# Kernel tuning notes

Hardware: AMD Instinct MI355X
Metric: run time of the kernel (lower is better)

## Reference

```python
import jax, jax.numpy as jnp
import numpy as np
import math

C = 256
NUM_CLASSES = 80
NUM_CONVS = 4
GROUPS = 32
LEVEL_SHAPES = [(100, 152), (50, 76), (25, 38), (13, 19), (7, 10)]
BATCH = 2


def conv2d(x, w, b):
    # x: [N,C,H,W], w: [O,I,3,3] -> SAME padding, stride 1
    y = jax.lax.conv_general_dilated(x, w, window_strides=(1, 1), padding='SAME',
                                     dimension_numbers=('NCHW', 'OIHW', 'NCHW'))
    return y + b[None, :, None, None]


def group_norm(x, w, b, groups=GROUPS, eps=1e-5):
    N, Ch, H, W = x.shape
    xg = x.reshape(N, groups, Ch // groups, H, W)
    mu = jnp.mean(xg, axis=(2, 3, 4), keepdims=True)
    var = jnp.var(xg, axis=(2, 3, 4), keepdims=True)
    xg = (xg - mu) * jax.lax.rsqrt(var + eps)
    x = xg.reshape(N, Ch, H, W)
    return x * w[None, :, None, None] + b[None, :, None, None]


def tower(x, cw, cb, gw, gb):
    for i in range(NUM_CONVS):
        x = jax.nn.relu(group_norm(conv2d(x, cw[i], cb[i]), gw[i], gb[i]))
    return x


def flatten_head(y, c):
    # [N, A*c, H, W] -> [N, H*W*A, c]  (matches view/permute/reshape in torch)
    N, AC, H, W = y.shape
    A = AC // c
    return y.reshape(N, A, c, H, W).transpose(0, 3, 4, 1, 2).reshape(N, H * W * A, c)


def setup_inputs() -> dict:
    key = jax.random.key(0)
    ks = iter(jax.random.split(key, 64))
    inp = {}
    for i, (h, w) in enumerate(LEVEL_SHAPES):
        inp[f"feat{i}"] = jax.random.normal(next(ks), (BATCH, C, h, w), jnp.float32)
    def cw(shape):  # conv weights init std=0.01 as in torch module
        return jax.random.normal(next(ks), shape, jnp.float32) * 0.01
    inp["cls_conv_w"] = cw((NUM_CONVS, C, C, 3, 3))
    inp["cls_conv_b"] = jnp.zeros((NUM_CONVS, C), jnp.float32)
    inp["cls_gn_w"] = jnp.ones((NUM_CONVS, C), jnp.float32)
    inp["cls_gn_b"] = jnp.zeros((NUM_CONVS, C), jnp.float32)
    inp["cls_out_w"] = cw((NUM_CLASSES, C, 3, 3))
    inp["cls_out_b"] = jnp.full((NUM_CLASSES,), -math.log(99.0), jnp.float32)  # prior prob 0.01
    inp["reg_conv_w"] = cw((NUM_CONVS, C, C, 3, 3))
    inp["reg_conv_b"] = jnp.zeros((NUM_CONVS, C), jnp.float32)
    inp["reg_gn_w"] = jnp.ones((NUM_CONVS, C), jnp.float32)
    inp["reg_gn_b"] = jnp.zeros((NUM_CONVS, C), jnp.float32)
    for name, oc in [("bbox", 4), ("ctr", 1), ("dim", 3), ("ori", 1), ("kp", 16), ("depth", 1)]:
        inp[f"{name}_w"] = cw((oc, C, 3, 3))
        inp[f"{name}_b"] = jnp.zeros((oc,), jnp.float32)
    return inp


def reference(feat0, feat1, feat2, feat3, feat4,
              cls_conv_w, cls_conv_b, cls_gn_w, cls_gn_b, cls_out_w, cls_out_b,
              reg_conv_w, reg_conv_b, reg_gn_w, reg_gn_b,
              bbox_w, bbox_b, ctr_w, ctr_b, dim_w, dim_b,
              ori_w, ori_b, kp_w, kp_b, depth_w, depth_b):
    feats = [feat0, feat1, feat2, feat3, feat4]
    cls_all, bbox_all, ctr_all, dim_all, ori_all, kp_all, depth_all = ([] for _ in range(7))
    for f in feats:
        cf = tower(f, cls_conv_w, cls_conv_b, cls_gn_w, cls_gn_b)
        cls_all.append(flatten_head(conv2d(cf, cls_out_w, cls_out_b), NUM_CLASSES))
        rf = tower(f, reg_conv_w, reg_conv_b, reg_gn_w, reg_gn_b)
        bbox_all.append(flatten_head(jax.nn.relu(conv2d(rf, bbox_w, bbox_b)), 4))
        ctr_all.append(flatten_head(conv2d(rf, ctr_w, ctr_b), 1))
        dim_all.append(flatten_head(conv2d(rf, dim_w, dim_b), 3))
        ori_all.append(flatten_head(conv2d(rf, ori_w, ori_b), 1))
        kp_all.append(flatten_head(conv2d(rf, kp_w, kp_b), 16))
        depth_all.append(flatten_head(conv2d(rf, depth_w, depth_b), 1))
    cat = lambda xs: jnp.concatenate(xs, axis=1)
    return (cat(cls_all), cat(bbox_all), cat(ctr_all), cat(dim_all),
            cat(ori_all), cat(kp_all), cat(depth_all))
```

## Files before the change

### kernel.cpp

```cpp
#include <hip/hip_runtime.h>
#include <stdint.h>

typedef unsigned short ushort_t;
typedef __bf16 bf16x8 __attribute__((ext_vector_type(8)));
typedef float f32x4 __attribute__((ext_vector_type(4)));

#define TOTAL_HW 20267
#define PTOT 21267

__constant__ int d_RB[26] = {3242720,3242720,3242720,3242720, 3404856, 3445390,3445390,3445390,
                             3566992, 3607526,3607526,3607526,3607526,3607526,3607526,3607526,3607526,
                             3607526,3607526,3607526,3607526,3607526,3607526,3607526,3607526, 4256070};
__constant__ int d_RM[26] = {4,4,4,4, 1, 3,3,3, 1, 16,16,16,16,16,16,16,16,16,16,16,16,16,16,16,16, 1};
__constant__ int d_RC[26] = {0,1,2,3, 0, 0,1,2, 0, 0,1,2,3,4,5,6,7,8,9,10,11,12,13,14,15, 0};

__constant__ int F_TC[6]   = {0,238,298,314,318,320};
__constant__ int F_TL[5]   = {119,30,8,2,1};
__constant__ int F_W[5]    = {152,76,38,19,10};
__constant__ int F_HW[5]   = {15200,3800,950,247,70};
__constant__ int F_PB[5]   = {0,15708,19764,20844,21159};
__constant__ int F_LOFF[5] = {0,15200,19000,19950,20197};
__constant__ int F_PC[6]   = {0,508,764,894,962,1000};
__constant__ int F_H[5]    = {100,50,25,13,7};

__device__ __forceinline__ ushort_t f2bf(float f) {
    union { float f; uint32_t i; } x; x.f = f;
    uint32_t r = x.i + 0x7fffu + ((x.i >> 16) & 1u);
    return (ushort_t)(r >> 16);
}
__device__ __forceinline__ float bf2f(ushort_t u) {
    union { uint32_t i; float f; } x; x.i = ((uint32_t)u) << 16; return x.f;
}
__device__ __forceinline__ void gld16(const ushort_t* g, ushort_t* lds) {
    __builtin_amdgcn_global_load_lds((const __attribute__((address_space(1))) void*)g,
                                     (__attribute__((address_space(3))) void*)lds, 16, 0, 0);
}

__global__ __launch_bounds__(256) void wtrans_towerall_k(const float* __restrict__ cw,
                                                         const float* __restrict__ rw,
                                                         ushort_t* __restrict__ dst)
{
    int id = blockIdx.x * 256 + threadIdx.x;
    int g = id >> 16;
    int oc = (id >> 8) & 255, ic = id & 255;
    const float* base = (g >= 4) ? rw : cw;
    int L = g & 3;
    const float* s = base + (size_t)L * 589824 + (size_t)(oc * 256 + ic) * 9;
    ushort_t* d = dst + (size_t)g * 589824 + oc * 256 + ic;
    #pragma unroll
    for (int t = 0; t < 9; t++) d[t * 65536] = f2bf(s[t]);
}
__global__ __launch_bounds__(256) void wtrans_cls_k(const float* __restrict__ src,
                                                    ushort_t* __restrict__ dst)
{
    int id = blockIdx.x * 256 + threadIdx.x;
    int oc = id >> 8, ic = id & 255;
    ushort_t* d = dst + oc * 256 + ic;
    if (oc < 80) {
        const float* s = src + (size_t)(oc * 256 + ic) * 9;
        #pragma unroll
        for (int t = 0; t < 9; t++) d[t * 32768] = f2bf(s[t]);
    } else {
        #pragma unroll
        for (int t = 0; t < 9; t++) d[t * 32768] = 0;
    }
}
__global__ __launch_bounds__(256) void wtrans_reg_k(
    const float* bbox_w, const float* ctr_w, const float* dim_w,
    const float* ori_w,  const float* kp_w,  const float* depth_w,
    const float* bbox_b, const float* ctr_b, const float* dim_b,
    const float* ori_b,  const float* kp_b,  const float* depth_b,
    ushort_t* __restrict__ dst, float* __restrict__ RegBias)
{
    int id = blockIdx.x * 256 + threadIdx.x;
    int oc = id >> 8, ic = id & 255;
    ushort_t* d = dst + oc * 256 + ic;
    if (oc < 26) {
        const float* s; int c;
        if (oc < 4)       { s = bbox_w;  c = oc; }
        else if (oc < 5)  { s = ctr_w;   c = 0; }
        else if (oc < 8)  { s = dim_w;   c = oc - 5; }
        else if (oc < 9)  { s = ori_w;   c = 0; }
        else if (oc < 25) { s = kp_w;    c = oc - 9; }
        else              { s = depth_w; c = 0; }
        const float* sp = s + (size_t)(c * 256 + ic) * 9;
        #pragma unroll
        for (int t = 0; t < 9; t++) d[t * 32768] = f2bf(sp[t]);
    } else {
        #pragma unroll
        for (int t = 0; t < 9; t++) d[t * 32768] = 0;
    }
    if (id < 26) {
        const float* b; int c;
        if (id < 4)       { b = bbox_b;  c = id; }
        else if (id < 5)  { b = ctr_b;   c = 0; }
        else if (id < 8)  { b = dim_b;   c = id - 5; }
        else if (id < 9)  { b = ori_b;   c = 0; }
        else if (id < 25) { b = kp_b;    c = id - 9; }
        else              { b = depth_b; c = 0; }
        RegBias[id] = b[c];
    }
}

__global__ __launch_bounds__(256) void pad_k(ushort_t* b0, ushort_t* b1, ushort_t* b2, ushort_t* b3)
{
    int u = blockIdx.x * 256 + threadIdx.x;
    if (u >= 256000) return;
    int chunk = u & 31; u >>= 5;
    int buf = u & 3; u >>= 2;
    int n = (u >= 1000) ? 1 : 0; int pidx = u - n * 1000;
    int l = 0;
    #pragma unroll
    for (int i = 1; i < 5; i++) if (pidx >= F_PC[i]) l = i;
    int q = pidx - F_PC[l];
    int W = F_W[l], H = F_H[l], Wp = W + 2;
    int py, px;
    if (q < Wp) { py = 0; px = q; }
    else if (q < 2 * Wp) { py = H + 1; px = q - Wp; }
    else { int q2 = q - 2 * Wp; py = 1 + (q2 >> 1); px = (q2 & 1) ? (Wp - 1) : 0; }
    ushort_t* base = b0;
    if (buf == 1) base = b1; else if (buf == 2) base = b2; else if (buf == 3) base = b3;
    *(uint4*)(base + ((size_t)n * PTOT + F_PB[l] + py * Wp + px) * 256 + chunk * 8) = uint4{0u,0u,0u,0u};
}

__global__ __launch_bounds__(256) void packF_k(
    const float* f0, const float* f1, const float* f2,
    const float* f3, const float* f4, ushort_t* __restrict__ S)
{
    __shared__ ushort_t tile[64][65];
    const int PCUM[6] = {0, 1904, 2384, 2504, 2536, 2552};
    const int PT[5]   = {238, 60, 15, 4, 2};
    int bid = blockIdx.x;
    int l = 0;
    #pragma unroll
    for (int i = 1; i < 5; i++) if (bid >= PCUM[i]) l = i;
    int r = bid - PCUM[l];
    int per_n = PT[l] * 4;
    int n = (r >= per_n) ? 1 : 0; r -= n * per_n;
    int pb = r >> 2, cb = r & 3;
    const float* fs = f0;
    if (l == 1) fs = f1; else if (l == 2) fs = f2; else if (l == 3) fs = f3; else if (l == 4) fs = f4;
    int HW = F_HW[l], W = F_W[l], Wp = W + 2;
    int p0 = pb * 64, c0 = cb * 64;
    int t = threadIdx.x;
    #pragma unroll
    for (int i = 0; i < 16; i++) {
        int idx = i * 256 + t; int cl = idx >> 6, pl = idx & 63;
        int p = p0 + pl; ushort_t v = 0;
        if (p < HW) v = f2bf(fs[(size_t)(n * 256 + c0 + cl) * HW + p]);
        tile[cl][pl] = v;
    }
    __syncthreads();
    ushort_t* ob = S + ((size_t)n * PTOT + F_PB[l]) * 256;
    #pragma unroll
    for (int i = 0; i < 16; i++) {
        int idx = i * 256 + t; int pl = idx >> 6, cl = idx & 63;
        int p = p0 + pl;
        if (p < HW) {
            int y = p / W, x = p - y * W;
            ob[((y + 1) * Wp + (x + 1)) * 256 + c0 + cl] = tile[cl][pl];
        }
    }
}

__global__ __launch_bounds__(512, 4) void convT_k(
    const ushort_t* __restrict__ srcC, const ushort_t* __restrict__ srcR,
    ushort_t* __restrict__ dstC, ushort_t* __restrict__ dstR,
    const ushort_t* __restrict__ wtAll,
    const float* __restrict__ biasC, const float* __restrict__ biasR,
    float* __restrict__ stats, int L)
{
    __shared__ __align__(16) ushort_t As[3][4096];
    __shared__ __align__(16) ushort_t Bs[3][4096];

    int gid = blockIdx.x;
    int xcd = gid & 7, idx = gid >> 3;
    int bid = xcd * 40 + (idx >> 2);
    int oc0 = (idx & 1) * 128;
    int tw = (idx >> 1) & 1;

    const ushort_t* src = tw ? srcR : srcC;
    ushort_t* dst = tw ? dstR : dstC;
    const ushort_t* wt = wtAll + (size_t)(tw * 4 + L) * 589824;
    const float* bias = (tw ? biasR : biasC) + L * 256;

    int l = 0;
    #pragma unroll
    for (int i = 1; i < 5; i++) if (bid >= F_TC[i]) l = i;
    int r = bid - F_TC[l];
    int tl = F_TL[l];
    int n = (r >= tl) ? 1 : 0; int tile = r - n * tl;
    int W = F_W[l], HW = F_HW[l], Wp = W + 2;
    int px0 = tile * 128;
    const ushort_t* sbase = src + ((size_t)n * PTOT + F_PB[l]) * 256;
    ushort_t* obase = dst + ((size_t)n * PTOT + F_PB[l]) * 256;

    int tid = threadIdx.x, wv = tid >> 6, ln = tid & 63;
    int wr = wv >> 2, wc = wv & 3;

    int aoff, boff;
    {
        int rloc = wv * 16 + (ln >> 2);
        int p = px0 + rloc; if (p > HW - 1) p = HW - 1;
        int y = p / W, x = p - y * W;
        int c = ((ln & 3) - (rloc >> 1)) & 3;
        aoff = ((y + 1) * Wp + (x + 1)) * 256 + c * 8;
        boff = (oc0 + rloc) * 256 + c * 8;
    }

    f32x4 acc[4][2];
    #pragma unroll
    for (int mi = 0; mi < 4; mi++)
        #pragma unroll
        for (int ni = 0; ni < 2; ni++) acc[mi][ni] = f32x4{0.f, 0.f, 0.f, 0.f};

    {
        int tapo = (-Wp - 1) * 256;
        gld16(sbase + aoff + tapo, &As[0][wv * 512]);
        gld16(wt + boff, &Bs[0][wv * 512]);
        asm volatile("" ::: "memory");
        gld16(sbase + aoff + tapo + 32, &As[1][wv * 512]);
        gld16(wt + 32 + boff, &Bs[1][wv * 512]);
    }

    #pragma unroll 3
    for (int it = 0; it < 72; ++it) {
        if (it < 71) {
            asm volatile("s_waitcnt vmcnt(2) lgkmcnt(0)\n\ts_barrier" ::: "memory");
        } else {
            asm volatile("s_waitcnt vmcnt(0) lgkmcnt(0)\n\ts_barrier" ::: "memory");
        }
        int nx = it + 2;
        if (nx < 72) {
            int tp = nx >> 3, kc = (nx & 7) << 5;
            int ky = tp / 3, kx = tp - ky * 3;
            int tapo = ((ky - 1) * Wp + (kx - 1)) * 256 + kc;
            const ushort_t* wtap = wt + tp * 65536 + kc;
            int bs = nx % 3;
            gld16(sbase + aoff + tapo, &As[bs][wv * 512]);
            gld16(wtap + boff, &Bs[bs][wv * 512]);
        }
        int b = it % 3;
        bf16x8 af[4], bg[2];
        #pragma unroll
        for (int mi = 0; mi < 4; mi++) {
            int rA = wr * 64 + mi * 16 + (ln & 15);
            int ch = ((ln >> 4) + (rA >> 1)) & 3;
            af[mi] = *(const bf16x8*)&As[b][rA * 32 + ch * 8];
        }
        #pragma unroll
        for (int ni = 0; ni < 2; ni++) {
            int rB = wc * 32 + ni * 16 + (ln & 15);
            int ch = ((ln >> 4) + (rB >> 1)) & 3;
            bg[ni] = *(const bf16x8*)&Bs[b][rB * 32 + ch * 8];
        }
        __builtin_amdgcn_s_setprio(1);
        #pragma unroll
        for (int mi = 0; mi < 4; mi++)
            #pragma unroll
            for (int ni = 0; ni < 2; ni++)
                acc[mi][ni] = __builtin_amdgcn_mfma_f32_16x16x32_bf16(af[mi], bg[ni], acc[mi][ni], 0, 0, 0);
        __builtin_amdgcn_s_setprio(0);
    }

    #pragma unroll
    for (int ni = 0; ni < 2; ni++) {
        int oc = oc0 + wc * 32 + ni * 16 + (ln & 15);
        float bv = bias[oc];
        float s = 0.f, q = 0.f;
        #pragma unroll
        for (int mi = 0; mi < 4; mi++) {
            int pb = px0 + wr * 64 + mi * 16 + ((ln >> 4) << 2);
            if (pb < HW) {
                int y = pb / W, x = pb - y * W;
                #pragma unroll
                for (int rr2 = 0; rr2 < 4; rr2++) {
                    int p = pb + rr2;
                    if (p < HW) {
                        float v = acc[mi][ni][rr2] + bv;
                        obase[((y + 1) * Wp + (x + 1)) * 256 + oc] = f2bf(v);
                        s += v; q += v * v;
                    }
                    x++; if (x == W) { x = 0; y++; }
                }
            }
        }
        s += __shfl_xor(s, 16, 64); q += __shfl_xor(q, 16, 64);
        s += __shfl_xor(s, 32, 64); q += __shfl_xor(q, 32, 64);
        s += __shfl_xor(s, 1, 64);  q += __shfl_xor(q, 1, 64);
        s += __shfl_xor(s, 2, 64);  q += __shfl_xor(q, 2, 64);
        s += __shfl_xor(s, 4, 64);  q += __shfl_xor(q, 4, 64);
        if (ln == 0 || ln == 8) {
            int g = (oc0 + wc * 32 + ni * 16 + (ln & 8)) >> 3;
            float* st = stats + (size_t)((tw * 4 + L) * 5 + l) * 128 + (n * 32 + g) * 2;
            atomicAdd(st, s); atomicAdd(st + 1, q);
        }
    }
}

__global__ __launch_bounds__(512, 4) void convH_k(
    const ushort_t* __restrict__ srcC, const ushort_t* __restrict__ srcR,
    const ushort_t* __restrict__ wtC, const ushort_t* __restrict__ wtR,
    const float* __restrict__ biasC, const float* __restrict__ biasR,
    float* __restrict__ outF)
{
    __shared__ __align__(16) ushort_t As[3][4096];
    __shared__ __align__(16) ushort_t Bs[3][4096];

    int gid = blockIdx.x;
    int xcd = gid & 7, idx = gid >> 3;
    int bid = xcd * 40 + (idx >> 1);
    int mode = idx & 1;

    const ushort_t* src = mode ? srcR : srcC;
    const ushort_t* wt  = mode ? wtR  : wtC;
    const float* bias   = mode ? biasR : biasC;

    int l = 0;
    #pragma unroll
    for (int i = 1; i < 5; i++) if (bid >= F_TC[i]) l = i;
    int r = bid - F_TC[l];
    int tl = F_TL[l];
    int n = (r >= tl) ? 1 : 0; int tile = r - n * tl;
    int W = F_W[l], HW = F_HW[l], Wp = W + 2;
    int px0 = tile * 128;
    const ushort_t* sbase = src + ((size_t)n * PTOT + F_PB[l]) * 256;

    int tid = threadIdx.x, wv = tid >> 6, ln = tid & 63;
    int wr = wv >> 2, wc = wv & 3;

    int aoff, boff;
    {
        int rloc = wv * 16 + (ln >> 2);
        int p = px0 + rloc; if (p > HW - 1) p = HW - 1;
        int y = p / W, x = p - y * W;
        int c = ((ln & 3) - (rloc >> 1)) & 3;
        aoff = ((y + 1) * Wp + (x + 1)) * 256 + c * 8;
        boff = rloc * 256 + c * 8;
    }

    f32x4 acc[4][2];
    #pragma unroll
    for (int mi = 0; mi < 4; mi++)
        #pragma unroll
        for (int ni = 0; ni < 2; ni++) acc[mi][ni] = f32x4{0.f, 0.f, 0.f, 0.f};

    {
        int tapo = (-Wp - 1) * 256;
        gld16(sbase + aoff + tapo, &As[0][wv * 512]);
        gld16(wt + boff, &Bs[0][wv * 512]);
        asm volatile("" ::: "memory");
        gld16(sbase + aoff + tapo + 32, &As[1][wv * 512]);
        gld16(wt + 32 + boff, &Bs[1][wv * 512]);
    }

    #pragma unroll 3
    for (int it = 0; it < 72; ++it) {
        if (it < 71) {
            asm volatile("s_waitcnt vmcnt(2) lgkmcnt(0)\n\ts_barrier" ::: "memory");
        } else {
            asm volatile("s_waitcnt vmcnt(0) lgkmcnt(0)\n\ts_barrier" ::: "memory");
        }
        int nx = it + 2;
        if (nx < 72) {
            int tp = nx >> 3, kc = (nx & 7) << 5;
            int ky = tp / 3, kx = tp - ky * 3;
            int tapo = ((ky - 1) * Wp + (kx - 1)) * 256 + kc;
            const ushort_t* wtap = wt + tp * 32768 + kc;
            int bs = nx % 3;
            gld16(sbase + aoff + tapo, &As[bs][wv * 512]);
            gld16(wtap + boff, &Bs[bs][wv * 512]);
        }
        int b = it % 3;
        bf16x8 af[4], bg[2];
        #pragma unroll
        for (int mi = 0; mi < 4; mi++) {
            int rA = wr * 64 + mi * 16 + (ln & 15);
            int ch = ((ln >> 4) + (rA >> 1)) & 3;
            af[mi] = *(const bf16x8*)&As[b][rA * 32 + ch * 8];
        }
        #pragma unroll
        for (int ni = 0; ni < 2; ni++) {
            int rB = wc * 32 + ni * 16 + (ln & 15);
            int ch = ((ln >> 4) + (rB >> 1)) & 3;
            bg[ni] = *(const bf16x8*)&Bs[b][rB * 32 + ch * 8];
        }
        __builtin_amdgcn_s_setprio(1);
        #pragma unroll
        for (int mi = 0; mi < 4; mi++)
            #pragma unroll
            for (int ni = 0; ni < 2; ni++)
                acc[mi][ni] = __builtin_amdgcn_mfma_f32_16x16x32_bf16(af[mi], bg[ni], acc[mi][ni], 0, 0, 0);
        __builtin_amdgcn_s_setprio(0);
    }

    #pragma unroll
    for (int ni = 0; ni < 2; ni++) {
        int oc = wc * 32 + ni * 16 + (ln & 15);
        bool valid = mode ? (oc < 26) : (oc < 80);
        if (valid) {
            float bv = bias[oc];
            int rb = 0, rm = 80, rc = oc; bool rl = false;
            if (mode) { rb = d_RB[oc]; rm = d_RM[oc]; rc = d_RC[oc]; rl = (oc < 4); }
            #pragma unroll
            for (int mi = 0; mi < 4; mi++) {
                int pb = px0 + wr * 64 + mi * 16 + ((ln >> 4) << 2);
                #pragma unroll
                for (int rr2 = 0; rr2 < 4; rr2++) {
                    int p = pb + rr2;
                    if (p < HW) {
                        float v = acc[mi][ni][rr2] + bv;
                        if (rl) v = fmaxf(v, 0.f);
                        int pg = n * TOTAL_HW + F_LOFF[l] + p;
                        outF[rb + (size_t)pg * rm + rc] = v;
                    }
                }
            }
        }
    }
}

__global__ __launch_bounds__(256) void normF_k(
    ushort_t* __restrict__ bufC, ushort_t* __restrict__ bufR,
    const float* __restrict__ stats,
    const float* __restrict__ gwC, const float* __restrict__ gwR,
    const float* __restrict__ gbC, const float* __restrict__ gbR, int L)
{
    int u = blockIdx.x * 256 + threadIdx.x;
    if (u >= 2594176) return;
    int tw = (u >= 1297088) ? 1 : 0; u -= tw * 1297088;
    int n = (u >= 648544) ? 1 : 0; u -= n * 648544;
    int cp = u >> 5, g = u & 31;
    int l = 0;
    #pragma unroll
    for (int i = 1; i < 5; i++) if (cp >= F_LOFF[i]) l = i;
    int p = cp - F_LOFF[l];
    int W = F_W[l], HW = F_HW[l];
    int y = p / W, x = p - y * W;
    const float* st = stats + (size_t)((tw * 4 + L) * 5 + l) * 128 + (n * 32 + g) * 2;
    float cnt = 8.0f * (float)HW;
    float mean = st[0] / cnt;
    float var = st[1] / cnt - mean * mean;
    float inv = rsqrtf(fmaxf(var, 0.f) + 1e-5f);
    const float* gw = (tw ? gwR : gwC) + L * 256 + g * 8;
    const float* gb = (tw ? gbR : gbC) + L * 256 + g * 8;
    ushort_t* buf = tw ? bufR : bufC;
    ushort_t* ptr = buf + (((size_t)n * PTOT + F_PB[l]) + (y + 1) * (W + 2) + (x + 1)) * 256 + g * 8;
    uint4 din = *(const uint4*)ptr;
    uint4 dout;
    const ushort_t* xi = (const ushort_t*)&din;
    ushort_t* oi = (ushort_t*)&dout;
    #pragma unroll
    for (int i = 0; i < 8; i++) {
        float v = (bf2f(xi[i]) - mean) * inv * gw[i] + gb[i];
        oi[i] = f2bf(fmaxf(v, 0.f));
    }
    *(uint4*)ptr = dout;
}


extern "C" void kernel_launch(void* const* d_in, const int* in_sizes, int n_in,
                              void* d_out, int out_size, void* d_ws, size_t ws_size,
                              hipStream_t stream) {
    const float* feats[5] = {(const float*)d_in[0], (const float*)d_in[1],
                             (const float*)d_in[2], (const float*)d_in[3],
                             (const float*)d_in[4]};
    const float* cls_conv_w = (const float*)d_in[5];
    const float* cls_conv_b = (const float*)d_in[6];
    const float* cls_gn_w   = (const float*)d_in[7];
    const float* cls_gn_b   = (const float*)d_in[8];
    const float* cls_out_w  = (const float*)d_in[9];
    const float* cls_out_b  = (const float*)d_in[10];
    const float* reg_conv_w = (const float*)d_in[11];
    const float* reg_conv_b = (const float*)d_in[12];
    const float* reg_gn_w   = (const float*)d_in[13];
    const float* reg_gn_b   = (const float*)d_in[14];

    char* wsb = (char*)d_ws;
    float* Stats     = (float*)wsb;
    float* RegBias   = (float*)(wsb + 20480);
    ushort_t* TowerWtAll = (ushort_t*)(wsb + 20608);
    ushort_t* WtCls  = (ushort_t*)(wsb + 9457792);
    ushort_t* WtReg  = (ushort_t*)(wsb + 10047616);
    ushort_t* S  = (ushort_t*)(wsb + 10637440);
    ushort_t* Ac = (ushort_t*)(wsb + 32414848);
    ushort_t* Ar = (ushort_t*)(wsb + 54192256);
    ushort_t* Br = (ushort_t*)(wsb + 75969664);
    float* outf  = (float*)d_out;

    hipMemsetAsync(d_ws, 0, 20608, stream);
    pad_k<<<1000, 256, 0, stream>>>(S, Ac, Ar, Br);

    wtrans_towerall_k<<<2048, 256, 0, stream>>>(cls_conv_w, reg_conv_w, TowerWtAll);
    wtrans_cls_k<<<128, 256, 0, stream>>>(cls_out_w, WtCls);
    wtrans_reg_k<<<128, 256, 0, stream>>>(
        (const float*)d_in[15], (const float*)d_in[17], (const float*)d_in[19],
        (const float*)d_in[21], (const float*)d_in[23], (const float*)d_in[25],
        (const float*)d_in[16], (const float*)d_in[18], (const float*)d_in[20],
        (const float*)d_in[22], (const float*)d_in[24], (const float*)d_in[26],
        WtReg, RegBias);

    packF_k<<<2552, 256, 0, stream>>>(feats[0], feats[1], feats[2], feats[3], feats[4], S);

    ushort_t* sc[4] = {S,  Ac, S,  Ac};
    ushort_t* dc[4] = {Ac, S,  Ac, S };
    ushort_t* sr[4] = {S,  Ar, Br, Ar};
    ushort_t* dr[4] = {Ar, Br, Ar, Br};
    for (int L = 0; L < 4; L++) {
        convT_k<<<1280, 512, 0, stream>>>(
            sc[L], sr[L], dc[L], dr[L], TowerWtAll, cls_conv_b, reg_conv_b, Stats, L);
        normF_k<<<10134, 256, 0, stream>>>(
            dc[L], dr[L], Stats, cls_gn_w, reg_gn_w, cls_gn_b, reg_gn_b, L);
    }
    convH_k<<<640, 512, 0, stream>>>(S, Br, WtCls, WtReg, cls_out_b, RegBias, outf);
}
```

Measured before the change: 890.3 us.

## Widen tower conv tile to 256 output channels with K=64 ping-pong stages

Each tower conv block now covers all 256 output channels (128x256 tile) instead of 128, which halves the grid and removes the duplicated activation loads across the two channel halves. The K step per stage grows to 64, and the loop is split into four MFMA phases, with global-to-LDS loads interleaved between barriers and raised priority around the math. LDS use rises to about 144KB per block, so launch bounds drop to 2 blocks per CU. This lowers occupancy and adds many barriers per iteration.

```diff
diff --git a/kernel.cpp b/kernel.cpp
--- a/kernel.cpp
+++ b/kernel.cpp
@@ -163,21 +163,20 @@
     }
 }
 
-__global__ __launch_bounds__(512, 4) void convT_k(
+__global__ __launch_bounds__(512, 2) void convT_k(
     const ushort_t* __restrict__ srcC, const ushort_t* __restrict__ srcR,
     ushort_t* __restrict__ dstC, ushort_t* __restrict__ dstR,
     const ushort_t* __restrict__ wtAll,
     const float* __restrict__ biasC, const float* __restrict__ biasR,
     float* __restrict__ stats, int L)
 {
-    __shared__ __align__(16) ushort_t As[3][4096];
-    __shared__ __align__(16) ushort_t Bs[3][4096];
+    __shared__ __align__(16) ushort_t As[3][8192];
+    __shared__ __align__(16) ushort_t Bs[3][16384];
 
     int gid = blockIdx.x;
     int xcd = gid & 7, idx = gid >> 3;
-    int bid = xcd * 40 + (idx >> 2);
-    int oc0 = (idx & 1) * 128;
-    int tw = (idx >> 1) & 1;
+    int bid = xcd * 40 + (idx >> 1);
+    int tw = idx & 1;
 
     const ushort_t* src = tw ? srcR : srcC;
     ushort_t* dst = tw ? dstR : dstC;
@@ -205,67 +204,123 @@
         int y = p / W, x = p - y * W;
         int c = ((ln & 3) - (rloc >> 1)) & 3;
         aoff = ((y + 1) * Wp + (x + 1)) * 256 + c * 8;
-        boff = (oc0 + rloc) * 256 + c * 8;
-    }
-
-    f32x4 acc[4][2];
+        boff = rloc * 256 + c * 8;
+    }
+
+    auto stA = [&](int kt, int bs) {
+        int tp = kt >> 2, kc0 = (kt & 3) << 6;
+        int ky = tp / 3, kx = tp - ky * 3;
+        int tapo = ((ky - 1) * Wp + (kx - 1)) * 256 + kc0;
+        gld16(sbase + aoff + tapo,      &As[bs][wv * 512]);
+        gld16(sbase + aoff + tapo + 32, &As[bs][4096 + wv * 512]);
+    };
+    auto stB0 = [&](int kt, int bs) {
+        int tp = kt >> 2, kc0 = (kt & 3) << 6;
+        const ushort_t* wb = wt + tp * 65536 + kc0 + boff;
+        gld16(wb,      &Bs[bs][wv * 512]);
+        gld16(wb + 32, &Bs[bs][8192 + wv * 512]);
+    };
+    auto stB1 = [&](int kt, int bs) {
+        int tp = kt >> 2, kc0 = (kt & 3) << 6;
+        const ushort_t* wb = wt + tp * 65536 + kc0 + 128 * 256 + boff;
+        gld16(wb,      &Bs[bs][4096 + wv * 512]);
+        gld16(wb + 32, &Bs[bs][8192 + 4096 + wv * 512]);
+    };
+    auto rdA = [&](int b, int kh, int mi) -> bf16x8 {
+        int rA = wr * 64 + mi * 16 + (ln & 15);
+        int ch = ((ln >> 4) + (rA >> 1)) & 3;
+        return *(const bf16x8*)&As[b][kh * 4096 + rA * 32 + ch * 8];
+    };
+    auto rdB = [&](int b, int kh, int ni) -> bf16x8 {
+        int rB = wc * 64 + ni * 16 + (ln & 15);
+        int ch = ((ln >> 4) + (rB >> 1)) & 3;
+        return *(const bf16x8*)&Bs[b][kh * 8192 + rB * 32 + ch * 8];
+    };
+
+    f32x4 acc[4][4];
     #pragma unroll
     for (int mi = 0; mi < 4; mi++)
         #pragma unroll
-        for (int ni = 0; ni < 2; ni++) acc[mi][ni] = f32x4{0.f, 0.f, 0.f, 0.f};
-
-    {
-        int tapo = (-Wp - 1) * 256;
-        gld16(sbase + aoff + tapo, &As[0][wv * 512]);
-        gld16(wt + boff, &Bs[0][wv * 512]);
-        asm volatile("" ::: "memory");
-        gld16(sbase + aoff + tapo + 32, &As[1][wv * 512]);
-        gld16(wt + 32 + boff, &Bs[1][wv * 512]);
-    }
+        for (int ni = 0; ni < 4; ni++) acc[mi][ni] = f32x4{0.f, 0.f, 0.f, 0.f};
+
+    stA(0, 0); stB0(0, 0); stB1(0, 0);
+    asm volatile("" ::: "memory");
+    stA(1, 1); stB0(1, 1); stB1(1, 1);
+    asm volatile("s_waitcnt vmcnt(6) lgkmcnt(0)\n\ts_barrier" ::: "memory");
 
     #pragma unroll 3
-    for (int it = 0; it < 72; ++it) {
-        if (it < 71) {
-            asm volatile("s_waitcnt vmcnt(2) lgkmcnt(0)\n\ts_barrier" ::: "memory");
+    for (int t = 0; t < 36; ++t) {
+        int bt = t % 3, ts = t + 2, bs = ts % 3;
+        bool st = (ts < 36);
+        bf16x8 a0[4], a1[4], p0[2], p1[2];
+
+        #pragma unroll
+        for (int mi = 0; mi < 4; mi++) a0[mi] = rdA(bt, 0, mi);
+        p0[0] = rdB(bt, 0, 0); p0[1] = rdB(bt, 0, 1);
+        if (st) stA(ts, bs);
+        asm volatile("s_barrier" ::: "memory");
+        asm volatile("s_waitcnt lgkmcnt(0)" ::: "memory");
+        __builtin_amdgcn_sched_barrier(0);
+        __builtin_amdgcn_s_setprio(1);
+        #pragma unroll
+        for (int mi = 0; mi < 4; mi++) {
+            acc[mi][0] = __builtin_amdgcn_mfma_f32_16x16x32_bf16(a0[mi], p0[0], acc[mi][0], 0, 0, 0);
+            acc[mi][1] = __builtin_amdgcn_mfma_f32_16x16x32_bf16(a0[mi], p0[1], acc[mi][1], 0, 0, 0);
+        }
+        __builtin_amdgcn_s_setprio(0);
+        asm volatile("s_barrier" ::: "memory");
+
+        p1[0] = rdB(bt, 0, 2); p1[1] = rdB(bt, 0, 3);
+        if (st) stB0(ts, bs);
+        asm volatile("s_barrier" ::: "memory");
+        asm volatile("s_waitcnt lgkmcnt(0)" ::: "memory");
+        __builtin_amdgcn_sched_barrier(0);
+        __builtin_amdgcn_s_setprio(1);
+        #pragma unroll
+        for (int mi = 0; mi < 4; mi++) {
+            acc[mi][2] = __builtin_amdgcn_mfma_f32_16x16x32_bf16(a0[mi], p1[0], acc[mi][2], 0, 0, 0);
+            acc[mi][3] = __builtin_amdgcn_mfma_f32_16x16x32_bf16(a0[mi], p1[1], acc[mi][3], 0, 0, 0);
+        }
+        __builtin_amdgcn_s_setprio(0);
+        asm volatile("s_barrier" ::: "memory");
+
+        #pragma unroll
+        for (int mi = 0; mi < 4; mi++) a1[mi] = rdA(bt, 1, mi);
+        p0[0] = rdB(bt, 1, 0); p0[1] = rdB(bt, 1, 1);
+        if (st) stB1(ts, bs);
+        asm volatile("s_barrier" ::: "memory");
+        asm volatile("s_waitcnt lgkmcnt(0)" ::: "memory");
+        __builtin_amdgcn_sched_barrier(0);
+        __builtin_amdgcn_s_setprio(1);
+        #pragma unroll
+        for (int mi = 0; mi < 4; mi++) {
+            acc[mi][0] = __builtin_amdgcn_mfma_f32_16x16x32_bf16(a1[mi], p0[0], acc[mi][0], 0, 0, 0);
+            acc[mi][1] = __builtin_amdgcn_mfma_f32_16x16x32_bf16(a1[mi], p0[1], acc[mi][1], 0, 0, 0);
+        }
+        __builtin_amdgcn_s_setprio(0);
+        asm volatile("s_barrier" ::: "memory");
+
+        p1[0] = rdB(bt, 1, 2); p1[1] = rdB(bt, 1, 3);
+        asm volatile("s_barrier" ::: "memory");
+        asm volatile("s_waitcnt lgkmcnt(0)" ::: "memory");
+        __builtin_amdgcn_sched_barrier(0);
+        __builtin_amdgcn_s_setprio(1);
+        #pragma unroll
+        for (int mi = 0; mi < 4; mi++) {
+            acc[mi][2] = __builtin_amdgcn_mfma_f32_16x16x32_bf16(a1[mi], p1[0], acc[mi][2], 0, 0, 0);
+            acc[mi][3] = __builtin_amdgcn_mfma_f32_16x16x32_bf16(a1[mi], p1[1], acc[mi][3], 0, 0, 0);
+        }
+        __builtin_amdgcn_s_setprio(0);
+        if (t < 34) {
+            asm volatile("s_waitcnt vmcnt(6) lgkmcnt(0)\n\ts_barrier" ::: "memory");
         } else {
             asm volatile("s_waitcnt vmcnt(0) lgkmcnt(0)\n\ts_barrier" ::: "memory");
         }
-        int nx = it + 2;
-        if (nx < 72) {
-            int tp = nx >> 3, kc = (nx & 7) << 5;
-            int ky = tp / 3, kx = tp - ky * 3;
-            int tapo = ((ky - 1) * Wp + (kx - 1)) * 256 + kc;
-            const ushort_t* wtap = wt + tp * 65536 + kc;
-            int bs = nx % 3;
-            gld16(sbase + aoff + tapo, &As[bs][wv * 512]);
-            gld16(wtap + boff, &Bs[bs][wv * 512]);
-        }
-        int b = it % 3;
-        bf16x8 af[4], bg[2];
-        #pragma unroll
-        for (int mi = 0; mi < 4; mi++) {
-            int rA = wr * 64 + mi * 16 + (ln & 15);
-            int ch = ((ln >> 4) + (rA >> 1)) & 3;
-            af[mi] = *(const bf16x8*)&As[b][rA * 32 + ch * 8];
-        }
-        #pragma unroll
-        for (int ni = 0; ni < 2; ni++) {
-            int rB = wc * 32 + ni * 16 + (ln & 15);
-            int ch = ((ln >> 4) + (rB >> 1)) & 3;
-            bg[ni] = *(const bf16x8*)&Bs[b][rB * 32 + ch * 8];
-        }
-        __builtin_amdgcn_s_setprio(1);
-        #pragma unroll
-        for (int mi = 0; mi < 4; mi++)
-            #pragma unroll
-            for (int ni = 0; ni < 2; ni++)
-                acc[mi][ni] = __builtin_amdgcn_mfma_f32_16x16x32_bf16(af[mi], bg[ni], acc[mi][ni], 0, 0, 0);
-        __builtin_amdgcn_s_setprio(0);
-    }
-
-    #pragma unroll
-    for (int ni = 0; ni < 2; ni++) {
-        int oc = oc0 + wc * 32 + ni * 16 + (ln & 15);
+    }
+
+    #pragma unroll
+    for (int ni = 0; ni < 4; ni++) {
+        int oc = wc * 64 + ni * 16 + (ln & 15);
         float bv = bias[oc];
         float s = 0.f, q = 0.f;
         #pragma unroll
@@ -291,7 +346,7 @@
         s += __shfl_xor(s, 2, 64);  q += __shfl_xor(q, 2, 64);
         s += __shfl_xor(s, 4, 64);  q += __shfl_xor(q, 4, 64);
         if (ln == 0 || ln == 8) {
-            int g = (oc0 + wc * 32 + ni * 16 + (ln & 8)) >> 3;
+            int g = (wc * 64 + ni * 16 + (ln & 8)) >> 3;
             float* st = stats + (size_t)((tw * 4 + L) * 5 + l) * 128 + (n * 32 + g) * 2;
             atomicAdd(st, s); atomicAdd(st + 1, q);
         }
@@ -507,7 +562,7 @@
     ushort_t* sr[4] = {S,  Ar, Br, Ar};
     ushort_t* dr[4] = {Ar, Br, Ar, Br};
     for (int L = 0; L < 4; L++) {
-        convT_k<<<1280, 512, 0, stream>>>(
+        convT_k<<<640, 512, 0, stream>>>(
             sc[L], sr[L], dc[L], dr[L], TowerWtAll, cls_conv_b, reg_conv_b, Stats, L);
         normF_k<<<10134, 256, 0, stream>>>(
             dc[L], dr[L], Stats, cls_gn_w, reg_gn_w, cls_gn_b, reg_gn_b, L);
```

Measured after the change: 971.2 us. +9.1%, slower.
